# Kernel optimization log

Measured on AMD Instinct MI355X. Metric: run time of the kernel, lower is better.

The kernel has to match this reference:

```python
import jax, jax.numpy as jnp
import numpy as np

N_NODES = 50000
N_EDGES = 640000
IN_F = 128
OUT_F = 32
HEADS = 4
ALPHA = 0.2  # leakyrelu negative slope


def setup_inputs() -> dict:
    key = jax.random.key(0)
    ks = jax.random.split(key, 9)
    xavier = lambda k, shape: jax.random.uniform(
        k, shape, jnp.float32, -1.0, 1.0) * (1.414 * np.sqrt(6.0 / (shape[0] + np.prod(shape[1:]))))
    return {
        "edge_index": jax.random.randint(ks[0], (2, N_EDGES), 0, N_NODES),
        "h": jax.random.normal(ks[1], (N_NODES, IN_F), jnp.float32),
        "edge_feat": jax.random.normal(ks[2], (N_EDGES, IN_F), jnp.float32),
        "W": xavier(ks[3], (IN_F, OUT_F * HEADS)),
        "W_e": xavier(ks[4], (IN_F, OUT_F * HEADS)),
        "a_src": xavier(ks[5], (1, HEADS, OUT_F)),
        "a_dst": xavier(ks[6], (1, HEADS, OUT_F)),
        "a_edge": xavier(ks[7], (1, HEADS, OUT_F)),
    }


def reference(edge_index, h, edge_feat, W, W_e, a_src, a_dst, a_edge):
    N = h.shape[0]
    Wh = (h @ W).reshape(N, HEADS, OUT_F)               # [N,H,D]
    We = (edge_feat @ W_e).reshape(-1, HEADS, OUT_F)    # [E,H,D]
    src, dst = edge_index[0], edge_index[1]
    Wh_src = Wh[src]                                    # [E,H,D] gather
    Wh_dst = Wh[dst]                                    # [E,H,D] gather
    e = ((Wh_src * a_src).sum(-1) + (Wh_dst * a_dst).sum(-1)
         + (We * a_edge).sum(-1))                       # [E,H]
    e = jnp.where(e >= 0, e, ALPHA * e)                 # leaky relu
    attention = jax.nn.softmax(e, axis=0)               # global softmax over edges (as in original)
    msg = attention[:, :, None] * Wh_src                # [E,H,D]
    h_prime = jax.ops.segment_sum(msg, dst, num_segments=N)  # scatter-add per dst
    h_prime = jax.nn.relu(h_prime)
    return h_prime.reshape(N, HEADS * OUT_F)
```

## Files before the change

kernel.cpp:

```cpp
#include <hip/hip_runtime.h>


typedef __attribute__((ext_vector_type(8))) short short8;
typedef __attribute__((ext_vector_type(4))) float f32x4;

#define ALPHA 0.2f
#define CAP 64

__device__ __forceinline__ unsigned short f2bf(float f) {
    unsigned u = __float_as_uint(f);
    u += 0x7fffu + ((u >> 16) & 1u);
    return (unsigned short)(u >> 16);
}
__device__ __forceinline__ float bf2f(unsigned short u) {
    return __uint_as_float(((unsigned)u) << 16);
}

__global__ void init_kernel(const float* __restrict__ We,
                            const float* __restrict__ a_edge,
                            float* __restrict__ Bfold,
                            int* __restrict__ cnt, int N) {
    if (blockIdx.x == 0) {
        if (threadIdx.x < 128) {
            int k = threadIdx.x;
            for (int h = 0; h < 4; h++) {
                float acc = 0.f;
                for (int d = 0; d < 32; d++)
                    acc += We[k * 128 + h * 32 + d] * a_edge[h * 32 + d];
                Bfold[k * 4 + h] = acc;
            }
        }
    } else {
        int nb = (int)gridDim.x - 1;
        int per = (N + nb - 1) / nb;
        int base = ((int)blockIdx.x - 1) * per;
        int end = base + per; if (end > N) end = N;
        for (int i = base + (int)threadIdx.x; i < end; i += (int)blockDim.x)
            cnt[i] = 0;
    }
}

__global__ __launch_bounds__(256) void gemm_wh(const float* __restrict__ hmat,
                                               const float* __restrict__ W,
                                               const float* __restrict__ a_src,
                                               const float* __restrict__ a_dst,
                                               unsigned short* __restrict__ Whb,
                                               float* __restrict__ s_src,
                                               float* __restrict__ s_dst, int N) {
    __shared__ short Wb[16384];
    int tid = threadIdx.x;
    for (int i = tid; i < 16384; i += 256) {
        int j = i & 7, lane = (i >> 3) & 63, ks = (i >> 9) & 3, nt = (i >> 11) & 7;
        int m = lane & 15, quad = lane >> 4;
        int k = ks * 32 + quad * 8 + j;
        int c = nt * 16 + m;
        Wb[i] = (short)f2bf(W[k * 128 + c]);
    }
    __syncthreads();
    int wave = tid >> 6, lane = tid & 63;
    int m = lane & 15, quad = lane >> 4;
    int row0 = blockIdx.x * 64 + wave * 16;
    int row = row0 + m;
    if (row >= N) row = N - 1;
    const float* hrow = hmat + (size_t)row * 128;
    short8 af[4];
    for (int ks = 0; ks < 4; ks++) {
        f32x4 lo = *(const f32x4*)(hrow + ks * 32 + quad * 8);
        f32x4 hi = *(const f32x4*)(hrow + ks * 32 + quad * 8 + 4);
        short8 a;
        a[0] = (short)f2bf(lo.x); a[1] = (short)f2bf(lo.y);
        a[2] = (short)f2bf(lo.z); a[3] = (short)f2bf(lo.w);
        a[4] = (short)f2bf(hi.x); a[5] = (short)f2bf(hi.y);
        a[6] = (short)f2bf(hi.z); a[7] = (short)f2bf(hi.w);
        af[ks] = a;
    }
    float ssrc[4] = {0.f, 0.f, 0.f, 0.f};
    float sdst[4] = {0.f, 0.f, 0.f, 0.f};
    for (int nt = 0; nt < 8; nt++) {
        f32x4 acc = {0.f, 0.f, 0.f, 0.f};
        for (int ks = 0; ks < 4; ks++) {
            short8 bf = *(const short8*)(Wb + ((nt * 4 + ks) * 64 + lane) * 8);
            acc = __builtin_amdgcn_mfma_f32_16x16x32_bf16(af[ks], bf, acc, 0, 0, 0);
        }
        float as = a_src[nt * 16 + m];
        float ad = a_dst[nt * 16 + m];
#pragma unroll
        for (int r = 0; r < 4; r++) {
            int orow = row0 + quad * 4 + r;
            if (orow < N) Whb[(size_t)orow * 128 + nt * 16 + m] = f2bf(acc[r]);
            ssrc[r] += acc[r] * as;
            sdst[r] += acc[r] * ad;
        }
        if (nt & 1) {
#pragma unroll
            for (int off = 1; off < 16; off <<= 1) {
#pragma unroll
                for (int r = 0; r < 4; r++) {
                    ssrc[r] += __shfl_xor(ssrc[r], off);
                    sdst[r] += __shfl_xor(sdst[r], off);
                }
            }
            if (m == 0) {
                int h = nt >> 1;
#pragma unroll
                for (int r = 0; r < 4; r++) {
                    int orow = row0 + quad * 4 + r;
                    if (orow < N) {
                        s_src[(size_t)orow * 4 + h] = ssrc[r];
                        s_dst[(size_t)orow * 4 + h] = sdst[r];
                    }
                }
            }
#pragma unroll
            for (int r = 0; r < 4; r++) { ssrc[r] = 0.f; sdst[r] = 0.f; }
        }
    }
}

__global__ __launch_bounds__(256) void edge_kernel(
        const int* __restrict__ ei, const float* __restrict__ ef,
        const float* __restrict__ Bfold, const float* __restrict__ s_src,
        const float* __restrict__ s_dst, int* __restrict__ cnt,
        int* __restrict__ bsrc, f32x4* __restrict__ bp,
        float* __restrict__ P, int E) {
    __shared__ float psh[16];
    int tid = threadIdx.x;
    long e = (long)blockIdx.x * 256 + tid;
    bool valid = e < E;
    float p0 = 0.f, p1 = 0.f, p2 = 0.f, p3 = 0.f;
    if (valid) {
        float a0 = 0.f, a1 = 0.f, a2 = 0.f, a3 = 0.f;
        const f32x4* xr = (const f32x4*)(ef + (size_t)e * 128);
        const f32x4* B4 = (const f32x4*)Bfold;
#pragma unroll 8
        for (int ch = 0; ch < 32; ch++) {
            f32x4 xv = xr[ch];
#pragma unroll
            for (int j = 0; j < 4; j++) {
                float xf = xv[j];
                f32x4 b = B4[ch * 4 + j];
                a0 += xf * b.x; a1 += xf * b.y; a2 += xf * b.z; a3 += xf * b.w;
            }
        }
        int srcn = ei[e];
        int dstn = ei[(size_t)E + e];
        f32x4 svs = ((const f32x4*)s_src)[srcn];
        f32x4 svd = ((const f32x4*)s_dst)[dstn];
        float t0 = a0 + svs.x + svd.x;
        float t1 = a1 + svs.y + svd.y;
        float t2 = a2 + svs.z + svd.z;
        float t3 = a3 + svs.w + svd.w;
        t0 = t0 >= 0.f ? t0 : ALPHA * t0;
        t1 = t1 >= 0.f ? t1 : ALPHA * t1;
        t2 = t2 >= 0.f ? t2 : ALPHA * t2;
        t3 = t3 >= 0.f ? t3 : ALPHA * t3;
        p0 = expf(t0); p1 = expf(t1); p2 = expf(t2); p3 = expf(t3);
        int pos = atomicAdd(&cnt[dstn], 1);
        if (pos < CAP) {
            size_t slot = (size_t)dstn * CAP + pos;
            bsrc[slot] = srcn;
            f32x4 pv = {p0, p1, p2, p3};
            bp[slot] = pv;
        }
    }
    float r0 = p0, r1 = p1, r2 = p2, r3 = p3;
#pragma unroll
    for (int off = 32; off > 0; off >>= 1) {
        r0 += __shfl_xor(r0, off);
        r1 += __shfl_xor(r1, off);
        r2 += __shfl_xor(r2, off);
        r3 += __shfl_xor(r3, off);
    }
    if ((tid & 63) == 0) {
        int w = tid >> 6;
        psh[w * 4 + 0] = r0; psh[w * 4 + 1] = r1;
        psh[w * 4 + 2] = r2; psh[w * 4 + 3] = r3;
    }
    __syncthreads();
    if (tid < 4)
        P[(size_t)blockIdx.x * 4 + tid] = psh[tid] + psh[4 + tid] + psh[8 + tid] + psh[12 + tid];
}

__global__ void reduce_sums(const float* __restrict__ P, float* __restrict__ sums, int nb) {
    __shared__ float red[256];
    int t = threadIdx.x;
    float acc = 0.f;
    for (int b = t >> 2; b < nb; b += 64) acc += P[(size_t)b * 4 + (t & 3)];
    red[t] = acc;
    __syncthreads();
    for (int s = 128; s >= 4; s >>= 1) {
        if (t < s) red[t] += red[t + s];
        __syncthreads();
    }
    if (t < 4) sums[t] = red[t];
}

__global__ __launch_bounds__(256) void agg_kernel(
        const int* __restrict__ cnt, const int* __restrict__ bsrc,
        const float* __restrict__ bp, const unsigned short* __restrict__ Whb,
        const float* __restrict__ sums, float* __restrict__ out, int N) {
    int wave = threadIdx.x >> 6, lane = threadIdx.x & 63;
    int n = blockIdx.x * 4 + wave;
    if (n >= N) return;
    int m = cnt[n]; if (m > CAP) m = CAP;
    size_t b0 = (size_t)n * CAP;
    int head = lane >> 4;
    float acc0 = 0.f, acc1 = 0.f;
    for (int i = 0; i < m; i++) {
        int src = bsrc[b0 + i];
        float ph = bp[(b0 + i) * 4 + head];
        unsigned w = *(const unsigned*)(Whb + (size_t)src * 128 + lane * 2);
        acc0 += ph * bf2f((unsigned short)(w & 0xffffu));
        acc1 += ph * bf2f((unsigned short)(w >> 16));
    }
    float inv = 1.0f / sums[head];
    float2 o;
    o.x = fmaxf(acc0, 0.f) * inv;
    o.y = fmaxf(acc1, 0.f) * inv;
    *(float2*)(out + (size_t)n * 128 + lane * 2) = o;
}

extern "C" void kernel_launch(void* const* d_in, const int* in_sizes, int n_in,
                              void* d_out, int out_size, void* d_ws, size_t ws_size,
                              hipStream_t stream) {
    const int* ei = (const int*)d_in[0];
    const float* hmat = (const float*)d_in[1];
    const float* ef = (const float*)d_in[2];
    const float* W = (const float*)d_in[3];
    const float* We = (const float*)d_in[4];
    const float* a_src = (const float*)d_in[5];
    const float* a_dst = (const float*)d_in[6];
    const float* a_edge = (const float*)d_in[7];
    int E = in_sizes[0] / 2;
    int N = in_sizes[1] / 128;
    int nEdgeBlocks = (E + 255) / 256;

    char* ws = (char*)d_ws;
    size_t off_b = 0;
    auto alloc = [&](size_t bytes) -> void* {
        void* p = ws + off_b;
        off_b = (off_b + bytes + 255) & ~(size_t)255;
        return p;
    };
    unsigned short* Whb = (unsigned short*)alloc((size_t)N * 128 * 2);
    float* s_src = (float*)alloc((size_t)N * 4 * 4);
    float* s_dst = (float*)alloc((size_t)N * 4 * 4);
    float* Bfold = (float*)alloc(128 * 4 * 4);
    int* cnt = (int*)alloc((size_t)N * 4);
    int* bsrc = (int*)alloc((size_t)N * CAP * 4);
    float* bp = (float*)alloc((size_t)N * CAP * 16);
    float* P = (float*)alloc((size_t)nEdgeBlocks * 4 * 4);
    float* sums = (float*)alloc(256);

    init_kernel<<<65, 256, 0, stream>>>(We, a_edge, Bfold, cnt, N);
    gemm_wh<<<(N + 63) / 64, 256, 0, stream>>>(hmat, W, a_src, a_dst, Whb, s_src, s_dst, N);
    edge_kernel<<<nEdgeBlocks, 256, 0, stream>>>(ei, ef, Bfold, s_src, s_dst,
                                                 cnt, bsrc, (f32x4*)bp, P, E);
    reduce_sums<<<1, 256, 0, stream>>>(P, sums, nEdgeBlocks);
    agg_kernel<<<(N + 3) / 4, 256, 0, stream>>>(cnt, bsrc, bp, Whb, sums,
                                                (float*)d_out, N);
}
```

Before: 607.8 us.

## Fuse init into GEMM, atomically reduce softmax sums, unroll aggregation gathers

Moves the counter zeroing and the Bfold fold into the Wh GEMM kernel and drops the separate reduce kernel, so per-block partial sums are added to a global sums buffer with atomics. That removes two launches. The aggregation kernel now preloads up to 32 bucket entries and issues their gathers together to raise memory-level parallelism, with a tail loop for larger buckets. Risks are a race on Bfold, which block 0 writes and the edge kernel reads (this relies on stream ordering and is fine), a nondeterministic float atomic summation order, and wasted gathers and register pressure for low-degree nodes.

```diff
diff --git a/kernel.cpp b/kernel.cpp
--- a/kernel.cpp
+++ b/kernel.cpp
@@ -6,6 +6,7 @@
 
 #define ALPHA 0.2f
 #define CAP 64
+#define UNR 32
 
 __device__ __forceinline__ unsigned short f2bf(float f) {
     unsigned u = __float_as_uint(f);
@@ -16,13 +17,24 @@
     return __uint_as_float(((unsigned)u) << 16);
 }
 
-__global__ void init_kernel(const float* __restrict__ We,
-                            const float* __restrict__ a_edge,
-                            float* __restrict__ Bfold,
-                            int* __restrict__ cnt, int N) {
+__global__ __launch_bounds__(256) void gemm_wh(const float* __restrict__ hmat,
+                                               const float* __restrict__ W,
+                                               const float* __restrict__ a_src,
+                                               const float* __restrict__ a_dst,
+                                               const float* __restrict__ We,
+                                               const float* __restrict__ a_edge,
+                                               float* __restrict__ Bfold,
+                                               int* __restrict__ cnt,
+                                               float* __restrict__ sums,
+                                               unsigned short* __restrict__ Whb,
+                                               float* __restrict__ s_src,
+                                               float* __restrict__ s_dst, int N) {
+    int tid = threadIdx.x;
+    for (int i = blockIdx.x * 256 + tid; i < N; i += (int)gridDim.x * 256)
+        cnt[i] = 0;
     if (blockIdx.x == 0) {
-        if (threadIdx.x < 128) {
-            int k = threadIdx.x;
+        if (tid < 128) {
+            int k = tid;
             for (int h = 0; h < 4; h++) {
                 float acc = 0.f;
                 for (int d = 0; d < 32; d++)
@@ -30,25 +42,9 @@
                 Bfold[k * 4 + h] = acc;
             }
         }
-    } else {
-        int nb = (int)gridDim.x - 1;
-        int per = (N + nb - 1) / nb;
-        int base = ((int)blockIdx.x - 1) * per;
-        int end = base + per; if (end > N) end = N;
-        for (int i = base + (int)threadIdx.x; i < end; i += (int)blockDim.x)
-            cnt[i] = 0;
-    }
-}
-
-__global__ __launch_bounds__(256) void gemm_wh(const float* __restrict__ hmat,
-                                               const float* __restrict__ W,
-                                               const float* __restrict__ a_src,
-                                               const float* __restrict__ a_dst,
-                                               unsigned short* __restrict__ Whb,
-                                               float* __restrict__ s_src,
-                                               float* __restrict__ s_dst, int N) {
+        if (tid < 4) sums[tid] = 0.f;
+    }
     __shared__ short Wb[16384];
-    int tid = threadIdx.x;
     for (int i = tid; i < 16384; i += 256) {
         int j = i & 7, lane = (i >> 3) & 63, ks = (i >> 9) & 3, nt = (i >> 11) & 7;
         int m = lane & 15, quad = lane >> 4;
@@ -122,7 +118,7 @@
         const float* __restrict__ Bfold, const float* __restrict__ s_src,
         const float* __restrict__ s_dst, int* __restrict__ cnt,
         int* __restrict__ bsrc, f32x4* __restrict__ bp,
-        float* __restrict__ P, int E) {
+        float* __restrict__ sums, int E) {
     __shared__ float psh[16];
     int tid = threadIdx.x;
     long e = (long)blockIdx.x * 256 + tid;
@@ -178,21 +174,7 @@
     }
     __syncthreads();
     if (tid < 4)
-        P[(size_t)blockIdx.x * 4 + tid] = psh[tid] + psh[4 + tid] + psh[8 + tid] + psh[12 + tid];
-}
-
-__global__ void reduce_sums(const float* __restrict__ P, float* __restrict__ sums, int nb) {
-    __shared__ float red[256];
-    int t = threadIdx.x;
-    float acc = 0.f;
-    for (int b = t >> 2; b < nb; b += 64) acc += P[(size_t)b * 4 + (t & 3)];
-    red[t] = acc;
-    __syncthreads();
-    for (int s = 128; s >= 4; s >>= 1) {
-        if (t < s) red[t] += red[t + s];
-        __syncthreads();
-    }
-    if (t < 4) sums[t] = red[t];
+        atomicAdd(&sums[tid], psh[tid] + psh[4 + tid] + psh[8 + tid] + psh[12 + tid]);
 }
 
 __global__ __launch_bounds__(256) void agg_kernel(
@@ -205,13 +187,36 @@
     int m = cnt[n]; if (m > CAP) m = CAP;
     size_t b0 = (size_t)n * CAP;
     int head = lane >> 4;
+    int sa[UNR];
+#pragma unroll
+    for (int g = 0; g < UNR / 4; g++) {
+        int4 v = *(const int4*)(bsrc + b0 + g * 4);
+        sa[g * 4 + 0] = v.x; sa[g * 4 + 1] = v.y;
+        sa[g * 4 + 2] = v.z; sa[g * 4 + 3] = v.w;
+    }
+    float qv[UNR];
+    unsigned wv[UNR];
+#pragma unroll
+    for (int s = 0; s < UNR; s++) {
+        float qraw = bp[(b0 + s) * 4 + head];
+        qv[s] = (s < m) ? qraw : 0.f;
+        int src = (s < m) ? sa[s] : 0;
+        wv[s] = *(const unsigned*)(Whb + (size_t)src * 128 + lane * 2);
+    }
     float acc0 = 0.f, acc1 = 0.f;
-    for (int i = 0; i < m; i++) {
-        int src = bsrc[b0 + i];
-        float ph = bp[(b0 + i) * 4 + head];
-        unsigned w = *(const unsigned*)(Whb + (size_t)src * 128 + lane * 2);
-        acc0 += ph * bf2f((unsigned short)(w & 0xffffu));
-        acc1 += ph * bf2f((unsigned short)(w >> 16));
+#pragma unroll
+    for (int s = 0; s < UNR; s++) {
+        acc0 += qv[s] * bf2f((unsigned short)(wv[s] & 0xffffu));
+        acc1 += qv[s] * bf2f((unsigned short)(wv[s] >> 16));
+    }
+    if (m > UNR) {
+        for (int i = UNR; i < m; i++) {
+            int src = bsrc[b0 + i];
+            float q = bp[(b0 + i) * 4 + head];
+            unsigned w = *(const unsigned*)(Whb + (size_t)src * 128 + lane * 2);
+            acc0 += q * bf2f((unsigned short)(w & 0xffffu));
+            acc1 += q * bf2f((unsigned short)(w >> 16));
+        }
     }
     float inv = 1.0f / sums[head];
     float2 o;
@@ -249,14 +254,12 @@
     int* cnt = (int*)alloc((size_t)N * 4);
     int* bsrc = (int*)alloc((size_t)N * CAP * 4);
     float* bp = (float*)alloc((size_t)N * CAP * 16);
-    float* P = (float*)alloc((size_t)nEdgeBlocks * 4 * 4);
     float* sums = (float*)alloc(256);
 
-    init_kernel<<<65, 256, 0, stream>>>(We, a_edge, Bfold, cnt, N);
-    gemm_wh<<<(N + 63) / 64, 256, 0, stream>>>(hmat, W, a_src, a_dst, Whb, s_src, s_dst, N);
+    gemm_wh<<<(N + 63) / 64, 256, 0, stream>>>(hmat, W, a_src, a_dst, We, a_edge,
+                                               Bfold, cnt, sums, Whb, s_src, s_dst, N);
     edge_kernel<<<nEdgeBlocks, 256, 0, stream>>>(ei, ef, Bfold, s_src, s_dst,
-                                                 cnt, bsrc, (f32x4*)bp, P, E);
-    reduce_sums<<<1, 256, 0, stream>>>(P, sums, nEdgeBlocks);
+                                                 cnt, bsrc, (f32x4*)bp, sums, E);
     agg_kernel<<<(N + 3) / 4, 256, 0, stream>>>(cnt, bsrc, bp, Whb, sums,
                                                 (float*)d_out, N);
 }
```

New measurement: 567.8 us. -6.6%, faster.
